# Optimization experiments

Measured on AMD Instinct MI355X. Metric: run time of the kernel, lower is better.

The kernel has to match this reference:

```python
import jax, jax.numpy as jnp
import numpy as np

VOCAB = 131072
EMB_DIM = 2048
N_PAD = 2048  # next power of two >= EMB_DIM
CB = 65536    # 2^16 codebook entries of E8 (8-dim) vectors


def fht(x):
    """Unnormalized fast Hadamard transform over the last dim (power of 2)."""
    n = x.shape[-1]
    orig = x.shape
    x = x.reshape(-1, n)
    h = 1
    while h < n:
        x = x.reshape(-1, n // (2 * h), 2, h)
        a, b = x[:, :, 0, :], x[:, :, 1, :]
        x = jnp.stack([a + b, a - b], axis=2).reshape(-1, n)
        h *= 2
    return x.reshape(orig)


def setup_inputs() -> dict:
    key = jax.random.key(0)
    k = jax.random.split(key, 6)
    input_ids = jax.random.randint(k[0], (8, 2048), 0, VOCAB, dtype=jnp.int32)
    Qidxs = jax.random.randint(k[1], (VOCAB, N_PAD // 8), -32768, 32768, dtype=jnp.int32).astype(jnp.int16)
    Qidxs2 = jax.random.randint(k[2], (VOCAB, N_PAD // 8), -32768, 32768, dtype=jnp.int32).astype(jnp.int16)
    codebook = (jax.random.normal(k[3], (CB, 8), dtype=jnp.float32) * 0.5).astype(jnp.float16)
    codebook2 = (jax.random.normal(k[4], (CB, 8), dtype=jnp.float32) * 0.5).astype(jnp.float16)
    SV = (jax.random.uniform(k[5], (N_PAD,), dtype=jnp.float32) * 0.5 + 0.75).astype(jnp.float16)
    Wscale = jnp.asarray(0.02, dtype=jnp.float32)
    inv_resid_scale = jnp.asarray(0.3, dtype=jnp.float32)
    return {"input_ids": input_ids, "Qidxs": Qidxs, "Qidxs2": Qidxs2,
            "codebook": codebook, "codebook2": codebook2, "SV": SV,
            "Wscale": Wscale, "inv_resid_scale": inv_resid_scale}


def reference(input_ids, Qidxs, Qidxs2, codebook, codebook2, SV, Wscale, inv_resid_scale):
    flat = input_ids.reshape(-1)                 # [N]
    n_tok = flat.shape[0]
    # stage 1: row gather -> packed int16 -> codebook gather
    rows1 = Qidxs[flat]                          # [N, N_PAD//8] int16
    idx1 = (rows1.astype(jnp.int32) & 0xFFFF).reshape(-1)
    deq = codebook[idx1].reshape(n_tok, N_PAD).astype(jnp.float32)
    # stage 2 residual
    rows2 = Qidxs2[flat]
    idx2 = (rows2.astype(jnp.int32) & 0xFFFF).reshape(-1)
    deq2 = codebook2[idx2].reshape(n_tok, N_PAD).astype(jnp.float32)
    deq = deq + deq2 * inv_resid_scale
    deq = deq * Wscale
    deq = fht(deq)
    deq = deq * SV.astype(jnp.float32)
    out = deq[:, :EMB_DIM].astype(jnp.float16)   # out dtype = SV.dtype
    return out.reshape(input_ids.shape + (EMB_DIM,))
```

## Files before the change

### kernel.cpp

```cpp
#include <hip/hip_runtime.h>
#include <hip/hip_fp16.h>

constexpr int WPB = 4;

typedef int   v4i __attribute__((ext_vector_type(4)));
typedef unsigned int v4u __attribute__((ext_vector_type(4)));

__global__ __launch_bounds__(256) void cvt_kernel(
    const float* __restrict__ cb1, const float* __restrict__ cb2,
    unsigned int* __restrict__ o1, unsigned int* __restrict__ o2)
{
    const int r = blockIdx.x * 256 + threadIdx.x;
    const float* src = (r < 65536) ? (cb1 + (size_t)r * 8)
                                   : (cb2 + (size_t)(r - 65536) * 8);
    unsigned int* dst = (r < 65536) ? (o1 + (size_t)r * 4)
                                    : (o2 + (size_t)(r - 65536) * 4);
    const float4 a = ((const float4*)src)[0];
    const float4 b = ((const float4*)src)[1];
    __half2 h0 = __floats2half2_rn(a.x, a.y);
    __half2 h1 = __floats2half2_rn(a.z, a.w);
    __half2 h2 = __floats2half2_rn(b.x, b.y);
    __half2 h3 = __floats2half2_rn(b.z, b.w);
    v4u o;
    o.x = *(unsigned int*)&h0; o.y = *(unsigned int*)&h1;
    o.z = *(unsigned int*)&h2; o.w = *(unsigned int*)&h3;
    *(v4u*)dst = o;
}

__global__ __launch_bounds__(256, 4) void e8rht_kernel_h(
    const int* __restrict__ input_ids,
    const int* __restrict__ Qidxs,
    const int* __restrict__ Qidxs2,
    const unsigned int* __restrict__ cb1h,
    const unsigned int* __restrict__ cb2h,
    const float* __restrict__ SV,
    const float* __restrict__ Wscale,
    const float* __restrict__ inv_resid,
    float* __restrict__ out)
{
    __shared__ __align__(16) float lds[WPB * 2048];
    const int wave = threadIdx.x >> 6;
    const int lane = threadIdx.x & 63;
    const int tok  = blockIdx.x * WPB + wave;

    const float ws  = Wscale[0];
    const float ws2 = ws * inv_resid[0];
    const int tid = input_ids[tok];

    const v4i q1 = __builtin_nontemporal_load((const v4i*)(Qidxs  + (size_t)tid * 256 + lane * 4));
    const v4i q2 = __builtin_nontemporal_load((const v4i*)(Qidxs2 + (size_t)tid * 256 + lane * 4));

    float v[32];
    {
        const int i1[4] = { q1.x & 0xFFFF, q1.y & 0xFFFF, q1.z & 0xFFFF, q1.w & 0xFFFF };
        const int i2[4] = { q2.x & 0xFFFF, q2.y & 0xFFFF, q2.z & 0xFFFF, q2.w & 0xFFFF };
        #pragma unroll
        for (int c = 0; c < 4; ++c) {
            const v4u a = *(const v4u*)(cb1h + (size_t)i1[c] * 4);
            const v4u b = *(const v4u*)(cb2h + (size_t)i2[c] * 4);
            const unsigned int au[4] = { a.x, a.y, a.z, a.w };
            const unsigned int bu[4] = { b.x, b.y, b.z, b.w };
            #pragma unroll
            for (int p = 0; p < 4; ++p) {
                const float2 fa = __half22float2(*(const __half2*)&au[p]);
                const float2 fb = __half22float2(*(const __half2*)&bu[p]);
                v[8*c + 2*p]     = fa.x * ws + fb.x * ws2;
                v[8*c + 2*p + 1] = fa.y * ws + fb.y * ws2;
            }
        }
    }

    #pragma unroll
    for (int h = 1; h < 32; h <<= 1) {
        #pragma unroll
        for (int r = 0; r < 32; ++r) {
            if ((r & h) == 0) {
                float a = v[r], b = v[r + h];
                v[r] = a + b;
                v[r + h] = a - b;
            }
        }
    }

    float* L = lds + wave * 2048;
    {
        const int t4 = lane >> 2, tl = lane & 3;
        #pragma unroll
        for (int j = 0; j < 32; ++j) {
            const int col = (((t4 ^ (j & 15)) << 2) | tl);
            L[(j << 6) + col] = v[j];
        }
    }
    __builtin_amdgcn_wave_barrier();

    const int j0 = lane >> 1;
    const int b  = lane & 1;
    float w[32];
    {
        const float4* Lr = (const float4*)(L + (j0 << 6));
        #pragma unroll
        for (int c = 0; c < 8; ++c) {
            const int ch = ((b << 3) + c) ^ (j0 & 15);
            const float4 f = Lr[ch];
            w[4*c + 0] = f.x; w[4*c + 1] = f.y; w[4*c + 2] = f.z; w[4*c + 3] = f.w;
        }
    }

    #pragma unroll
    for (int h = 1; h < 32; h <<= 1) {
        #pragma unroll
        for (int r = 0; r < 32; ++r) {
            if ((r & h) == 0) {
                float a = w[r], bb = w[r + h];
                w[r] = a + bb;
                w[r + h] = a - bb;
            }
        }
    }

    #pragma unroll
    for (int r = 0; r < 32; ++r) {
        const float o = __shfl_xor(w[r], 1, 64);
        w[r] = b ? (o - w[r]) : (w[r] + o);
    }

    const size_t obase = (size_t)tok * 2048;
    const int ebase = (b << 10) | j0;
    #pragma unroll
    for (int r = 0; r < 32; ++r) {
        const int e = ebase + (r << 5);
        __builtin_nontemporal_store(w[r] * SV[e], &out[obase + e]);
    }
}

__global__ __launch_bounds__(256, 4) void e8rht_kernel_f(
    const int* __restrict__ input_ids,
    const int* __restrict__ Qidxs,
    const int* __restrict__ Qidxs2,
    const float* __restrict__ codebook,
    const float* __restrict__ codebook2,
    const float* __restrict__ SV,
    const float* __restrict__ Wscale,
    const float* __restrict__ inv_resid,
    float* __restrict__ out)
{
    __shared__ __align__(16) float lds[WPB * 2048];
    const int wave = threadIdx.x >> 6;
    const int lane = threadIdx.x & 63;
    const int tok  = blockIdx.x * WPB + wave;

    const float ws  = Wscale[0];
    const float ws2 = ws * inv_resid[0];
    const int tid = input_ids[tok];

    const int4 q1 = *(const int4*)(Qidxs  + (size_t)tid * 256 + lane * 4);
    const int4 q2 = *(const int4*)(Qidxs2 + (size_t)tid * 256 + lane * 4);

    float v[32];
    {
        const int i1[4] = { q1.x & 0xFFFF, q1.y & 0xFFFF, q1.z & 0xFFFF, q1.w & 0xFFFF };
        const int i2[4] = { q2.x & 0xFFFF, q2.y & 0xFFFF, q2.z & 0xFFFF, q2.w & 0xFFFF };
        #pragma unroll
        for (int c = 0; c < 4; ++c) {
            const float4* r1 = (const float4*)(codebook  + (size_t)i1[c] * 8);
            const float4* r2 = (const float4*)(codebook2 + (size_t)i2[c] * 8);
            const float4 a0 = r1[0], a1 = r1[1];
            const float4 b0 = r2[0], b1 = r2[1];
            v[8*c+0]=a0.x*ws+b0.x*ws2; v[8*c+1]=a0.y*ws+b0.y*ws2;
            v[8*c+2]=a0.z*ws+b0.z*ws2; v[8*c+3]=a0.w*ws+b0.w*ws2;
            v[8*c+4]=a1.x*ws+b1.x*ws2; v[8*c+5]=a1.y*ws+b1.y*ws2;
            v[8*c+6]=a1.z*ws+b1.z*ws2; v[8*c+7]=a1.w*ws+b1.w*ws2;
        }
    }
    #pragma unroll
    for (int h = 1; h < 32; h <<= 1)
        #pragma unroll
        for (int r = 0; r < 32; ++r)
            if ((r & h) == 0) { float a=v[r],b=v[r+h]; v[r]=a+b; v[r+h]=a-b; }

    float* L = lds + wave * 2048;
    {
        const int t4 = lane >> 2, tl = lane & 3;
        #pragma unroll
        for (int j = 0; j < 32; ++j)
            L[(j << 6) + (((t4 ^ (j & 15)) << 2) | tl)] = v[j];
    }
    __syncthreads();
    const int j0 = lane >> 1;
    const int b  = lane & 1;
    float w[32];
    {
        const float4* Lr = (const float4*)(L + (j0 << 6));
        #pragma unroll
        for (int c = 0; c < 8; ++c) {
            const float4 f = Lr[((b << 3) + c) ^ (j0 & 15)];
            w[4*c+0]=f.x; w[4*c+1]=f.y; w[4*c+2]=f.z; w[4*c+3]=f.w;
        }
    }
    #pragma unroll
    for (int h = 1; h < 32; h <<= 1)
        #pragma unroll
        for (int r = 0; r < 32; ++r)
            if ((r & h) == 0) { float a=w[r],bb=w[r+h]; w[r]=a+bb; w[r+h]=a-bb; }
    #pragma unroll
    for (int r = 0; r < 32; ++r) {
        const float o = __shfl_xor(w[r], 1, 64);
        w[r] = b ? (o - w[r]) : (w[r] + o);
    }
    const size_t obase = (size_t)tok * 2048;
    const int ebase = (b << 10) | j0;
    #pragma unroll
    for (int r = 0; r < 32; ++r) {
        const int e = ebase + (r << 5);
        out[obase + e] = w[r] * SV[e];
    }
}

extern "C" void kernel_launch(void* const* d_in, const int* in_sizes, int n_in,
                              void* d_out, int out_size, void* d_ws, size_t ws_size,
                              hipStream_t stream) {
    const int* input_ids   = (const int*)d_in[0];
    const int* Qidxs       = (const int*)d_in[1];
    const int* Qidxs2      = (const int*)d_in[2];
    const float* codebook  = (const float*)d_in[3];
    const float* codebook2 = (const float*)d_in[4];
    const float* SV        = (const float*)d_in[5];
    const float* wscale    = (const float*)d_in[6];
    const float* irs       = (const float*)d_in[7];
    float* out             = (float*)d_out;

    const int n_tok = in_sizes[0];
    const int grid  = n_tok / WPB;

    const size_t cb_h_bytes = (size_t)65536 * 8 * 2;
    if (ws_size >= 2 * cb_h_bytes) {
        unsigned int* cb1h = (unsigned int*)d_ws;
        unsigned int* cb2h = (unsigned int*)((char*)d_ws + cb_h_bytes);
        cvt_kernel<<<512, 256, 0, stream>>>(codebook, codebook2, cb1h, cb2h);
        e8rht_kernel_h<<<grid, 256, 0, stream>>>(input_ids, Qidxs, Qidxs2,
                                                 cb1h, cb2h, SV, wscale, irs, out);
    } else {
        e8rht_kernel_f<<<grid, 256, 0, stream>>>(input_ids, Qidxs, Qidxs2,
                                                 codebook, codebook2, SV,
                                                 wscale, irs, out);
    }
}
```

Baseline: 318.6 us.

## Process two tokens per wave with software-pipelined codebook gathers

Each wave now handles two tokens. The second token's row loads and codebook gathers are issued before the first token's Hadamard transform and store, so gather latency overlaps compute. SV loads are also hoisted ahead of the second FHT stage. The grid is halved, and register pressure goes up to hold the in-flight gathers, which could cut occupancy.

```diff
diff --git a/kernel.cpp b/kernel.cpp
--- a/kernel.cpp
+++ b/kernel.cpp
@@ -2,6 +2,7 @@
 #include <hip/hip_fp16.h>
 
 constexpr int WPB = 4;
+constexpr int TPW = 2;
 
 typedef int   v4i __attribute__((ext_vector_type(4)));
 typedef unsigned int v4u __attribute__((ext_vector_type(4)));
@@ -27,6 +28,97 @@
     *(v4u*)dst = o;
 }
 
+__device__ __forceinline__ void issue_gathers(const v4i q1, const v4i q2,
+    const unsigned int* __restrict__ cb1h, const unsigned int* __restrict__ cb2h,
+    v4u g1[4], v4u g2[4])
+{
+    const int i1[4] = { q1.x & 0xFFFF, q1.y & 0xFFFF, q1.z & 0xFFFF, q1.w & 0xFFFF };
+    const int i2[4] = { q2.x & 0xFFFF, q2.y & 0xFFFF, q2.z & 0xFFFF, q2.w & 0xFFFF };
+    #pragma unroll
+    for (int c = 0; c < 4; ++c) g1[c] = *(const v4u*)(cb1h + (size_t)i1[c] * 4);
+    #pragma unroll
+    for (int c = 0; c < 4; ++c) g2[c] = *(const v4u*)(cb2h + (size_t)i2[c] * 4);
+}
+
+__device__ __forceinline__ void convert8(const v4u g1[4], const v4u g2[4],
+    const float ws, const float ws2, float v[32])
+{
+    #pragma unroll
+    for (int c = 0; c < 4; ++c) {
+        const unsigned int au[4] = { g1[c].x, g1[c].y, g1[c].z, g1[c].w };
+        const unsigned int bu[4] = { g2[c].x, g2[c].y, g2[c].z, g2[c].w };
+        #pragma unroll
+        for (int p = 0; p < 4; ++p) {
+            const float2 fa = __half22float2(*(const __half2*)&au[p]);
+            const float2 fb = __half22float2(*(const __half2*)&bu[p]);
+            v[8*c + 2*p]     = fa.x * ws + fb.x * ws2;
+            v[8*c + 2*p + 1] = fa.y * ws + fb.y * ws2;
+        }
+    }
+}
+
+__device__ __forceinline__ void process_tok(float v[32], float* __restrict__ L,
+    const int lane, const float* __restrict__ SV, float* __restrict__ outp)
+{
+    #pragma unroll
+    for (int h = 1; h < 32; h <<= 1) {
+        #pragma unroll
+        for (int r = 0; r < 32; ++r) {
+            if ((r & h) == 0) { float a = v[r], b = v[r + h]; v[r] = a + b; v[r + h] = a - b; }
+        }
+    }
+
+    __builtin_amdgcn_wave_barrier();
+    {
+        const int t4 = lane >> 2, tl = lane & 3;
+        #pragma unroll
+        for (int j = 0; j < 32; ++j) {
+            const int col = (((t4 ^ (j & 15)) << 2) | tl);
+            L[(j << 6) + col] = v[j];
+        }
+    }
+    __builtin_amdgcn_wave_barrier();
+
+    const int j0 = lane >> 1;
+    const int b  = lane & 1;
+    float w[32];
+    {
+        const float4* Lr = (const float4*)(L + (j0 << 6));
+        #pragma unroll
+        for (int c = 0; c < 8; ++c) {
+            const int ch = ((b << 3) + c) ^ (j0 & 15);
+            const float4 f = Lr[ch];
+            w[4*c + 0] = f.x; w[4*c + 1] = f.y; w[4*c + 2] = f.z; w[4*c + 3] = f.w;
+        }
+    }
+    __builtin_amdgcn_wave_barrier();
+
+    const int ebase = (b << 10) | j0;
+    float svv[32];
+    #pragma unroll
+    for (int r = 0; r < 32; ++r) svv[r] = SV[ebase + (r << 5)];
+
+    #pragma unroll
+    for (int h = 1; h < 32; h <<= 1) {
+        #pragma unroll
+        for (int r = 0; r < 32; ++r) {
+            if ((r & h) == 0) { float a = w[r], bb = w[r + h]; w[r] = a + bb; w[r + h] = a - bb; }
+        }
+    }
+
+    #pragma unroll
+    for (int r = 0; r < 32; ++r) {
+        const float o = __shfl_xor(w[r], 1, 64);
+        w[r] = b ? (o - w[r]) : (w[r] + o);
+    }
+
+    #pragma unroll
+    for (int r = 0; r < 32; ++r) {
+        const int e = ebase + (r << 5);
+        __builtin_nontemporal_store(w[r] * svv[r], &outp[e]);
+    }
+}
+
 __global__ __launch_bounds__(256, 4) void e8rht_kernel_h(
     const int* __restrict__ input_ids,
     const int* __restrict__ Qidxs,
@@ -41,96 +133,30 @@
     __shared__ __align__(16) float lds[WPB * 2048];
     const int wave = threadIdx.x >> 6;
     const int lane = threadIdx.x & 63;
-    const int tok  = blockIdx.x * WPB + wave;
+    const int tokA = (blockIdx.x * WPB + wave) * TPW;
+    const int tokB = tokA + 1;
 
     const float ws  = Wscale[0];
     const float ws2 = ws * inv_resid[0];
-    const int tid = input_ids[tok];
-
-    const v4i q1 = __builtin_nontemporal_load((const v4i*)(Qidxs  + (size_t)tid * 256 + lane * 4));
-    const v4i q2 = __builtin_nontemporal_load((const v4i*)(Qidxs2 + (size_t)tid * 256 + lane * 4));
-
+    const int tidA = input_ids[tokA];
+    const int tidB = input_ids[tokB];
+
+    const v4i q1A = __builtin_nontemporal_load((const v4i*)(Qidxs  + (size_t)tidA * 256 + lane * 4));
+    const v4i q2A = __builtin_nontemporal_load((const v4i*)(Qidxs2 + (size_t)tidA * 256 + lane * 4));
+    const v4i q1B = __builtin_nontemporal_load((const v4i*)(Qidxs  + (size_t)tidB * 256 + lane * 4));
+    const v4i q2B = __builtin_nontemporal_load((const v4i*)(Qidxs2 + (size_t)tidB * 256 + lane * 4));
+
+    v4u g1[4], g2[4];
     float v[32];
-    {
-        const int i1[4] = { q1.x & 0xFFFF, q1.y & 0xFFFF, q1.z & 0xFFFF, q1.w & 0xFFFF };
-        const int i2[4] = { q2.x & 0xFFFF, q2.y & 0xFFFF, q2.z & 0xFFFF, q2.w & 0xFFFF };
-        #pragma unroll
-        for (int c = 0; c < 4; ++c) {
-            const v4u a = *(const v4u*)(cb1h + (size_t)i1[c] * 4);
-            const v4u b = *(const v4u*)(cb2h + (size_t)i2[c] * 4);
-            const unsigned int au[4] = { a.x, a.y, a.z, a.w };
-            const unsigned int bu[4] = { b.x, b.y, b.z, b.w };
-            #pragma unroll
-            for (int p = 0; p < 4; ++p) {
-                const float2 fa = __half22float2(*(const __half2*)&au[p]);
-                const float2 fb = __half22float2(*(const __half2*)&bu[p]);
-                v[8*c + 2*p]     = fa.x * ws + fb.x * ws2;
-                v[8*c + 2*p + 1] = fa.y * ws + fb.y * ws2;
-            }
-        }
-    }
-
-    #pragma unroll
-    for (int h = 1; h < 32; h <<= 1) {
-        #pragma unroll
-        for (int r = 0; r < 32; ++r) {
-            if ((r & h) == 0) {
-                float a = v[r], b = v[r + h];
-                v[r] = a + b;
-                v[r + h] = a - b;
-            }
-        }
-    }
-
     float* L = lds + wave * 2048;
-    {
-        const int t4 = lane >> 2, tl = lane & 3;
-        #pragma unroll
-        for (int j = 0; j < 32; ++j) {
-            const int col = (((t4 ^ (j & 15)) << 2) | tl);
-            L[(j << 6) + col] = v[j];
-        }
-    }
-    __builtin_amdgcn_wave_barrier();
-
-    const int j0 = lane >> 1;
-    const int b  = lane & 1;
-    float w[32];
-    {
-        const float4* Lr = (const float4*)(L + (j0 << 6));
-        #pragma unroll
-        for (int c = 0; c < 8; ++c) {
-            const int ch = ((b << 3) + c) ^ (j0 & 15);
-            const float4 f = Lr[ch];
-            w[4*c + 0] = f.x; w[4*c + 1] = f.y; w[4*c + 2] = f.z; w[4*c + 3] = f.w;
-        }
-    }
-
-    #pragma unroll
-    for (int h = 1; h < 32; h <<= 1) {
-        #pragma unroll
-        for (int r = 0; r < 32; ++r) {
-            if ((r & h) == 0) {
-                float a = w[r], bb = w[r + h];
-                w[r] = a + bb;
-                w[r + h] = a - bb;
-            }
-        }
-    }
-
-    #pragma unroll
-    for (int r = 0; r < 32; ++r) {
-        const float o = __shfl_xor(w[r], 1, 64);
-        w[r] = b ? (o - w[r]) : (w[r] + o);
-    }
-
-    const size_t obase = (size_t)tok * 2048;
-    const int ebase = (b << 10) | j0;
-    #pragma unroll
-    for (int r = 0; r < 32; ++r) {
-        const int e = ebase + (r << 5);
-        __builtin_nontemporal_store(w[r] * SV[e], &out[obase + e]);
-    }
+
+    issue_gathers(q1A, q2A, cb1h, cb2h, g1, g2);
+    convert8(g1, g2, ws, ws2, v);
+    issue_gathers(q1B, q2B, cb1h, cb2h, g1, g2);
+    process_tok(v, L, lane, SV, out + (size_t)tokA * 2048);
+
+    convert8(g1, g2, ws, ws2, v);
+    process_tok(v, L, lane, SV, out + (size_t)tokB * 2048);
 }
 
 __global__ __launch_bounds__(256, 4) void e8rht_kernel_f(
@@ -230,16 +256,17 @@
     float* out             = (float*)d_out;
 
     const int n_tok = in_sizes[0];
-    const int grid  = n_tok / WPB;
 
     const size_t cb_h_bytes = (size_t)65536 * 8 * 2;
     if (ws_size >= 2 * cb_h_bytes) {
         unsigned int* cb1h = (unsigned int*)d_ws;
         unsigned int* cb2h = (unsigned int*)((char*)d_ws + cb_h_bytes);
         cvt_kernel<<<512, 256, 0, stream>>>(codebook, codebook2, cb1h, cb2h);
+        const int grid = n_tok / (WPB * TPW);
         e8rht_kernel_h<<<grid, 256, 0, stream>>>(input_ids, Qidxs, Qidxs2,
                                                  cb1h, cb2h, SV, wscale, irs, out);
     } else {
+        const int grid = n_tok / WPB;
         e8rht_kernel_f<<<grid, 256, 0, stream>>>(input_ids, Qidxs, Qidxs2,
                                                  codebook, codebook2, SV,
                                                  wscale, irs, out);
```

Measured after the change: 317.0 us. Within noise of the previous version (-0.5%).
